# Performance work log

Measured on AMD Instinct MI355X. Metric: run time of the kernel, lower is better.

The kernel has to match this reference:

```python
import jax, jax.numpy as jnp
import numpy as np

N, C, E, H = 50000, 128, 1_600_000, 32
JITTER = 1e-20


def _lin(k, fan_in, fan_out):
    return jax.random.normal(k, (fan_in, fan_out), jnp.float32) / np.sqrt(fan_in)


def setup_inputs() -> dict:
    key = jax.random.key(0)
    ks = jax.random.split(key, 20)
    x = jax.random.normal(ks[0], (N, C), jnp.float32)
    edge_index = jax.random.randint(ks[1], (2, E), 0, N, dtype=jnp.int64)
    inp = {"x": x, "edge_index": edge_index}
    # actor params
    inp["aW"] = _lin(ks[2], C, C); inp["ab"] = jnp.zeros((C,), jnp.float32)
    inp["a1W"] = _lin(ks[3], C, H); inp["a1b"] = jnp.zeros((H,), jnp.float32)
    inp["a2W"] = _lin(ks[4], H, H); inp["a2b"] = jnp.zeros((H,), jnp.float32)
    inp["a3W"] = _lin(ks[5], H, 2); inp["a3b"] = jnp.zeros((2,), jnp.float32)
    # critic params
    inp["cW"] = _lin(ks[6], C, C); inp["cb"] = jnp.zeros((C,), jnp.float32)
    inp["c1W"] = _lin(ks[7], C, H); inp["c1b"] = jnp.zeros((H,), jnp.float32)
    inp["c2W"] = _lin(ks[8], H, H); inp["c2b"] = jnp.zeros((H,), jnp.float32)
    inp["c3W"] = _lin(ks[9], H, 2); inp["c3b"] = jnp.zeros((2,), jnp.float32)
    return inp


def gcn_conv(x, src, dst, W, b):
    """Standard PyG GCNConv: add self-loops, symmetric degree norm, X@W, scatter-add, +bias."""
    n = x.shape[0]
    loop = jnp.arange(n)
    s = jnp.concatenate([src, loop])  # [E+N]
    d = jnp.concatenate([dst, loop])
    deg = jax.ops.segment_sum(jnp.ones_like(d, jnp.float32), d, num_segments=n)
    dinv = jnp.where(deg > 0, jax.lax.rsqrt(deg), 0.0)
    norm = dinv[s] * dinv[d]                     # [E+N]
    h = x @ W                                    # [N, C]
    agg = jax.ops.segment_sum(h[s] * norm[:, None], d, num_segments=n)
    return agg + b


def reference(x, edge_index, aW, ab, a1W, a1b, a2W, a2b, a3W, a3b,
              cW, cb, c1W, c1b, c2W, c2b, c3W, c3b):
    src, dst = edge_index[0], edge_index[1]
    # actor
    h = jax.nn.relu(gcn_conv(x, src, dst, aW, ab)) + x
    h = jax.nn.relu(h @ a1W + a1b)
    h = jax.nn.relu(h @ a2W + a2b)
    a = h @ a3W + a3b                            # [N, 2]
    concentration = jax.nn.softplus(a[:, 0]) + JITTER
    p = jax.nn.softplus(a[:, 1])
    action2_probs = p / jnp.sum(p)
    # critic
    hc = jax.nn.relu(gcn_conv(x, src, dst, cW, cb)) + x
    hc = jnp.sum(hc, axis=0)                     # [C]
    hc = jax.nn.relu(hc @ c1W + c1b)
    hc = jax.nn.relu(hc @ c2W + c2b)
    value = hc @ c3W + c3b                       # [2]
    return (concentration, value, action2_probs)
```

## Files before the change

kernel.cpp:

```cpp
#include <hip/hip_runtime.h>
#include <hip/hip_bf16.h>
#include <hip/hip_fp16.h>
#include <math.h>

#define C 128
#define BCAP 12288

using half8x = __attribute__((ext_vector_type(8))) _Float16;
using half4x = __attribute__((ext_vector_type(4))) _Float16;
using f32x4  = __attribute__((ext_vector_type(4))) float;

__device__ inline float4 h4_to_f4(uint2 u) {
    __half2 p0 = *(__half2*)&u.x;
    __half2 p1 = *(__half2*)&u.y;
    float2 f0 = __half22float2(p0), f1 = __half22float2(p1);
    return make_float4(f0.x, f0.y, f1.x, f1.y);
}

__device__ inline float softplusf(float v) {
    return (v > 20.f) ? v : log1pf(expf(v));
}

__global__ __launch_bounds__(256) void initk(unsigned* gcur, float* colsum, float* pSum) {
    int t = threadIdx.x;
    gcur[t] = 0u;
    if (t < 128) colsum[t] = 0.f;
    if (t == 128) pSum[0] = 0.f;
}

__global__ __launch_bounds__(256) void wtk(const float* __restrict__ aW, const float* __restrict__ cW,
                                           const float* __restrict__ a1W,
                                           __half* __restrict__ wt, __half* __restrict__ a1wt) {
    int idx = blockIdx.x * 256 + threadIdx.x;
    if (idx < 32768) {
        int y = idx >> 14, r = idx & 16383;
        int k = r >> 7, n = r & 127;
        const float* W = y ? cW : aW;
        wt[((size_t)y << 14) + n * 128 + k] = __float2half(W[k * 128 + n]);
    } else if (idx < 36864) {
        int r = idx - 32768;
        int k = r >> 5, n = r & 31;
        a1wt[n * 128 + k] = __float2half(a1W[k * 32 + n]);
    }
}

__global__ __launch_bounds__(256) void bink(const int* __restrict__ ei,
                                            unsigned* __restrict__ gcur,
                                            unsigned* __restrict__ gstage,
                                            int E, int NBKT) {
    __shared__ unsigned raw[6400];
    __shared__ unsigned image[6400];
    __shared__ unsigned cnt[256];
    __shared__ unsigned pref[256];
    __shared__ unsigned cur[256];
    __shared__ unsigned gb[256];
    int t = threadIdx.x, b = blockIdx.x;
    int elo = (int)((long long)b * E / 256);
    int ehi = (int)((long long)(b + 1) * E / 256);
    int n = ehi - elo;

    for (int i = t; i < n; i += 256) {
        int d = __builtin_nontemporal_load(ei + E + elo + i);
        int s = __builtin_nontemporal_load(ei + elo + i);
        raw[i] = (unsigned)s | ((unsigned)(d & 255) << 16) | ((unsigned)(d >> 8) << 24);
    }
    cnt[t] = 0u; cur[t] = 0u;
    __syncthreads();
    for (int i = t; i < n; i += 256) atomicAdd(&cnt[raw[i] >> 24], 1u);
    __syncthreads();
    pref[t] = cnt[t];
    __syncthreads();
    for (int off = 1; off < 256; off <<= 1) {
        unsigned add = (t >= off) ? pref[t - off] : 0u;
        __syncthreads();
        pref[t] += add;
        __syncthreads();
    }
    gb[t] = (t < NBKT && cnt[t]) ? atomicAdd(&gcur[t], cnt[t]) : 0u;
    __syncthreads();
    for (int i = t; i < n; i += 256) {
        unsigned v = raw[i];
        unsigned B = v >> 24;
        unsigned pos = (pref[B] - cnt[B]) + atomicAdd(&cur[B], 1u);
        image[pos] = v & 0xFFFFFFu;
    }
    __syncthreads();
    int wv = t >> 6, lane = t & 63;
    for (int B = wv; B < NBKT; B += 4) {
        unsigned c = cnt[B];
        if (!c) continue;
        unsigned eb = pref[B] - c;
        unsigned gbase = gb[B];
        unsigned c2 = (gbase < BCAP) ? ((c < BCAP - gbase) ? c : BCAP - gbase) : 0u;
        for (unsigned i = lane; i < c2; i += 64)
            gstage[(size_t)B * BCAP + gbase + i] = image[eb + i];
    }
}

__global__ void bktscank(const unsigned* __restrict__ gcur, unsigned* __restrict__ bktbase, int NBKT) {
    __shared__ unsigned tmp[256];
    int t = threadIdx.x;
    unsigned g = (t < NBKT) ? gcur[t] : 0u;
    unsigned v = (g < BCAP) ? g : BCAP;
    tmp[t] = v;
    __syncthreads();
    for (int off = 1; off < 256; off <<= 1) {
        unsigned add = (t >= off) ? tmp[t - off] : 0u;
        __syncthreads();
        tmp[t] += add;
        __syncthreads();
    }
    if (t < NBKT) bktbase[t] = tmp[t] - v;
}

__global__ __launch_bounds__(256) void placek(const unsigned* __restrict__ gstage,
                                              const unsigned* __restrict__ gcur,
                                              const unsigned* __restrict__ bktbase,
                                              int* __restrict__ rowptr, float* __restrict__ dinv,
                                              int* __restrict__ col, int N, int NBKT) {
    __shared__ unsigned image[BCAP];
    __shared__ unsigned cnt[256];
    __shared__ unsigned pref[256];
    __shared__ unsigned cur[256];
    int B = blockIdx.x, t = threadIdx.x;
    unsigned g = gcur[B];
    unsigned m = (g < BCAP) ? g : BCAP;
    unsigned base = bktbase[B];
    const unsigned* st = gstage + (size_t)B * BCAP;

    cnt[t] = 0u; cur[t] = 0u;
    __syncthreads();
    for (unsigned i = t; i < m; i += 256) atomicAdd(&cnt[(st[i] >> 16) & 255u], 1u);
    __syncthreads();
    pref[t] = cnt[t];
    __syncthreads();
    for (int off = 1; off < 256; off <<= 1) {
        unsigned add = (t >= off) ? pref[t - off] : 0u;
        __syncthreads();
        pref[t] += add;
        __syncthreads();
    }
    int d = B * 256 + t;
    if (d < N) {
        rowptr[d] = (int)(base + pref[t] - cnt[t]);
        dinv[d] = rsqrtf((float)(cnt[t] + 1u));
    }
    if (B == NBKT - 1 && t == 0) rowptr[N] = (int)(base + m);
    for (unsigned i = t; i < m; i += 256) {
        unsigned v = st[i];
        unsigned dl = (v >> 16) & 255u;
        unsigned pos = (pref[dl] - cnt[dl]) + atomicAdd(&cur[dl], 1u);
        image[pos] = v & 0xFFFFu;
    }
    __syncthreads();
    for (unsigned i = t; i < m; i += 256) col[base + i] = (int)image[i];
}

__global__ __launch_bounds__(256) void xhk(const float* __restrict__ x, const float* __restrict__ dinv,
                                           __half* __restrict__ xh, __half* __restrict__ x16, int N) {
    int i = blockIdx.x * 256 + threadIdx.x;
    if (i >= N * 64) return;
    int node = i >> 6, fp = (i & 63) * 2;
    float w = dinv[node];
    float2 f = *(const float2*)&x[(size_t)node * C + fp];
    __half2 h = __floats2half2_rn(f.x * w, f.y * w);
    __half2 hx = __floats2half2_rn(f.x, f.y);
    *(unsigned*)&xh[(size_t)node * C + fp] = *(unsigned*)&h;
    *(unsigned*)&x16[(size_t)node * C + fp] = *(unsigned*)&hx;
}

__global__ __launch_bounds__(256) void gatherk(const int* __restrict__ col,
                                               const int* __restrict__ rowptr,
                                               const __half* __restrict__ xh,
                                               const float* __restrict__ dinv,
                                               __half* __restrict__ gg, int N) {
    __shared__ int snb[4][64];
    int t = threadIdx.x;
    int wid = t >> 6, lane = t & 63;
    int d = blockIdx.x * 4 + wid;
    if (d >= N) return;
    int beg = rowptr[d], end = rowptr[d + 1];
    int half = lane >> 5, sub = lane & 31;
    int f = sub * 4;

    float a0 = 0.f, a1 = 0.f, a2 = 0.f, a3 = 0.f;

    for (int c = beg; c < end; c += 64) {
        if (c + lane < end) snb[wid][lane] = col[c + lane];
        int n = end - c; if (n > 64) n = 64;
        int j = 0;
        for (; j + 3 < n; j += 4) {
            size_t i0 = (size_t)snb[wid][j + half] * C + f;
            size_t i1 = (size_t)snb[wid][j + 2 + half] * C + f;
            float4 v0 = h4_to_f4(*(const uint2*)&xh[i0]);
            float4 v1 = h4_to_f4(*(const uint2*)&xh[i1]);
            a0 += v0.x + v1.x;
            a1 += v0.y + v1.y;
            a2 += v0.z + v1.z;
            a3 += v0.w + v1.w;
        }
        for (; j < n; j += 2) {
            if (j + half < n) {
                float4 v = h4_to_f4(*(const uint2*)&xh[(size_t)snb[wid][j + half] * C + f]);
                a0 += v.x; a1 += v.y; a2 += v.z; a3 += v.w;
            }
        }
    }
    a0 += __shfl_xor(a0, 32, 64);
    a1 += __shfl_xor(a1, 32, 64);
    a2 += __shfl_xor(a2, 32, 64);
    a3 += __shfl_xor(a3, 32, 64);

    if (half == 0) {
        float4 s4 = h4_to_f4(*(const uint2*)&xh[(size_t)d * C + f]);
        float dv = dinv[d];
        __half2 h0 = __floats2half2_rn((a0 + s4.x) * dv, (a1 + s4.y) * dv);
        __half2 h1 = __floats2half2_rn((a2 + s4.z) * dv, (a3 + s4.w) * dv);
        uint2 u; u.x = *(unsigned*)&h0; u.y = *(unsigned*)&h1;
        *(uint2*)&gg[(size_t)d * C + f] = u;
    }
}

__global__ __launch_bounds__(256) void gemm2k(const __half* __restrict__ gg,
                                              const __half* __restrict__ wt,
                                              const __half* __restrict__ a1wt,
                                              const float* __restrict__ ab, const float* __restrict__ cb,
                                              const __half* __restrict__ x16,
                                              const float* __restrict__ a1b,
                                              const float* __restrict__ a2W, const float* __restrict__ a2b,
                                              const float* __restrict__ a3W, const float* __restrict__ a3b,
                                              float* __restrict__ scratch,
                                              float* __restrict__ out, float* __restrict__ pSum, int N) {
    __shared__ char As[16384];
    __shared__ char Act[16384];
    __shared__ char Aux[8448];
    _Float16* w2t = (_Float16*)Aux;
    _Float16* h1b = (_Float16*)(Aux + 2560);
    float* w3s    = (float*)(Aux + 7680);
    float* scol   = (float*)(Aux + 7936);

    const int row0 = blockIdx.x * 64;
    const int t = threadIdx.x;

#pragma unroll
    for (int i = 0; i < 4; ++i) {
        int c = t + i * 256;
        int row = c >> 4, cb16 = (c & 15) * 16;
        int grow = row0 + row;
        uint4 u = make_uint4(0u, 0u, 0u, 0u);
        if (grow < N) u = *(const uint4*)&gg[(size_t)grow * C + (c & 15) * 8];
        *(uint4*)(As + row * 256 + (cb16 ^ ((row & 7) << 4))) = u;
    }
#pragma unroll
    for (int i = 0; i < 4; ++i) {
        int idx = t + i * 256;
        int k = idx >> 5, n = idx & 31;
        w2t[n * 40 + k] = (_Float16)a2W[idx];
    }
    if (t < 64) w3s[t] = a3W[t];
    __syncthreads();

    int wv = t >> 6, l = t & 63;
    int lm = l & 15, lk = l >> 4;
    int koffB = lk * 16;
    int koffH = lk * 8;

    const __half* WA = wt;
    const __half* WC = wt + 16384;

#pragma unroll
    for (int nc2 = 0; nc2 < 2; ++nc2) {
        const int nc = wv * 2 + nc2;
        const __half* wpA = WA + (nc * 16 + lm) * 128;
        const __half* wpC = WC + (nc * 16 + lm) * 128;
        half8x bfA[4], bfC[4];
#pragma unroll
        for (int kc = 0; kc < 4; ++kc) {
            bfA[kc] = *(const half8x*)(wpA + kc * 32 + koffH);
            bfC[kc] = *(const half8x*)(wpC + kc * 32 + koffH);
        }
        float4 bvA = *(const float4*)&ab[nc * 16 + lk * 4];
        float4 bvC = *(const float4*)&cb[nc * 16 + lk * 4];
        float v0 = 0.f, v1 = 0.f, v2 = 0.f, v3 = 0.f;

#pragma unroll
        for (int rg = 0; rg < 4; ++rg) {
            int rowA = rg * 16 + lm;
            int grow = row0 + rowA;
            bool valid = grow < N;
            int sw = (rowA & 7) << 4;
            const char* rp = As + rowA * 256;
            f32x4 accA = {0.f, 0.f, 0.f, 0.f};
            f32x4 accC = {0.f, 0.f, 0.f, 0.f};
#pragma unroll
            for (int kc = 0; kc < 4; ++kc) {
                half8x afr = *(const half8x*)(rp + ((kc * 64 + koffB) ^ sw));
                accA = __builtin_amdgcn_mfma_f32_16x16x32_f16(bfA[kc], afr, accA, 0, 0, 0);
                accC = __builtin_amdgcn_mfma_f32_16x16x32_f16(bfC[kc], afr, accC, 0, 0, 0);
            }
            half4x xq = {};
            if (valid) xq = *(const half4x*)&x16[(size_t)grow * C + nc * 16 + lk * 4];
            half4x hv = { (_Float16)(valid ? fmaxf(accA[0] + bvA.x, 0.f) + (float)xq[0] : 0.f),
                          (_Float16)(valid ? fmaxf(accA[1] + bvA.y, 0.f) + (float)xq[1] : 0.f),
                          (_Float16)(valid ? fmaxf(accA[2] + bvA.z, 0.f) + (float)xq[2] : 0.f),
                          (_Float16)(valid ? fmaxf(accA[3] + bvA.w, 0.f) + (float)xq[3] : 0.f) };
            *(half4x*)(Act + rowA * 256 + ((nc * 32 + lk * 8) ^ sw)) = hv;
            v0 += valid ? fmaxf(accC[0] + bvC.x, 0.f) + (float)xq[0] : 0.f;
            v1 += valid ? fmaxf(accC[1] + bvC.y, 0.f) + (float)xq[1] : 0.f;
            v2 += valid ? fmaxf(accC[2] + bvC.z, 0.f) + (float)xq[2] : 0.f;
            v3 += valid ? fmaxf(accC[3] + bvC.w, 0.f) + (float)xq[3] : 0.f;
        }
        v0 += __shfl_xor(v0, 1, 64); v0 += __shfl_xor(v0, 2, 64);
        v0 += __shfl_xor(v0, 4, 64); v0 += __shfl_xor(v0, 8, 64);
        v1 += __shfl_xor(v1, 1, 64); v1 += __shfl_xor(v1, 2, 64);
        v1 += __shfl_xor(v1, 4, 64); v1 += __shfl_xor(v1, 8, 64);
        v2 += __shfl_xor(v2, 1, 64); v2 += __shfl_xor(v2, 2, 64);
        v2 += __shfl_xor(v2, 4, 64); v2 += __shfl_xor(v2, 8, 64);
        v3 += __shfl_xor(v3, 1, 64); v3 += __shfl_xor(v3, 2, 64);
        v3 += __shfl_xor(v3, 4, 64); v3 += __shfl_xor(v3, 8, 64);
        if (lm == 0)
            *(float4*)&scol[nc * 16 + lk * 4] = make_float4(v0, v1, v2, v3);
    }
    __syncthreads();

    if (t < 128)
        scratch[(size_t)blockIdx.x * 128 + t] = scol[t];

    const int rowM = wv * 16 + lm;
    const int growM = row0 + rowM;
    const bool validM = growM < N;
    const int swM = (rowM & 7) << 4;

    half8x a1f[4];
    {
        const char* rp = Act + rowM * 256;
#pragma unroll
        for (int kc = 0; kc < 4; ++kc)
            a1f[kc] = *(const half8x*)(rp + ((kc * 64 + koffB) ^ swM));
    }
#pragma unroll
    for (int ct = 0; ct < 2; ++ct) {
        const __half* ap = a1wt + (ct * 16 + lm) * 128;
        f32x4 acc1 = {0.f, 0.f, 0.f, 0.f};
#pragma unroll
        for (int kc = 0; kc < 4; ++kc) {
            half8x bq = *(const half8x*)(ap + kc * 32 + koffH);
            acc1 = __builtin_amdgcn_mfma_f32_16x16x32_f16(bq, a1f[kc], acc1, 0, 0, 0);
        }
        float4 b1v = *(const float4*)&a1b[ct * 16 + lk * 4];
        half4x h = { (_Float16)fmaxf(acc1[0] + b1v.x, 0.f),
                     (_Float16)fmaxf(acc1[1] + b1v.y, 0.f),
                     (_Float16)fmaxf(acc1[2] + b1v.z, 0.f),
                     (_Float16)fmaxf(acc1[3] + b1v.w, 0.f) };
        *(half4x*)((char*)h1b + rowM * 80 + ct * 32 + lk * 8) = h;
    }

    half4x alo = *(const half4x*)((char*)h1b + rowM * 80 + lk * 16);
    half4x ahi = *(const half4x*)((char*)h1b + rowM * 80 + lk * 16 + 8);
    half8x a2f = __builtin_shufflevector(alo, ahi, 0, 1, 2, 3, 4, 5, 6, 7);
    float p0 = 0.f, p1 = 0.f;
#pragma unroll
    for (int ct = 0; ct < 2; ++ct) {
        half4x blo = *(const half4x*)((char*)w2t + (ct * 16 + lm) * 80 + lk * 16);
        half4x bhi = *(const half4x*)((char*)w2t + (ct * 16 + lm) * 80 + lk * 16 + 8);
        half8x b2f = __builtin_shufflevector(blo, bhi, 0, 1, 2, 3, 4, 5, 6, 7);
        f32x4 acc2 = {0.f, 0.f, 0.f, 0.f};
        acc2 = __builtin_amdgcn_mfma_f32_16x16x32_f16(b2f, a2f, acc2, 0, 0, 0);
        float4 b2v = *(const float4*)&a2b[ct * 16 + lk * 4];
#pragma unroll
        for (int j = 0; j < 4; ++j) {
            int f = ct * 16 + lk * 4 + j;
            float h2v = fmaxf(acc2[j] + (&b2v.x)[j], 0.f);
            float2 w3 = *(const float2*)&w3s[f * 2];
            p0 += h2v * w3.x;
            p1 += h2v * w3.y;
        }
    }
    p0 += __shfl_xor(p0, 16, 64); p0 += __shfl_xor(p0, 32, 64);
    p1 += __shfl_xor(p1, 16, 64); p1 += __shfl_xor(p1, 32, 64);
    float wave_psum = 0.f;
    if (lk == 0 && validM) {
        float s0 = softplusf(p0 + a3b[0]);
        float s1 = softplusf(p1 + a3b[1]);
        out[growM] = s0 + 1e-20f;
        out[(size_t)N + 2 + growM] = s1;
        wave_psum = s1;
    }
    wave_psum += __shfl_xor(wave_psum, 1, 64);
    wave_psum += __shfl_xor(wave_psum, 2, 64);
    wave_psum += __shfl_xor(wave_psum, 4, 64);
    wave_psum += __shfl_xor(wave_psum, 8, 64);
    wave_psum += __shfl_xor(wave_psum, 16, 64);
    wave_psum += __shfl_xor(wave_psum, 32, 64);
    if (l == 0) atomicAdd(pSum, wave_psum);
}

__global__ __launch_bounds__(128) void csredk(const float* __restrict__ scratch, float* __restrict__ colsum, int nblk) {
    int t = threadIdx.x;
    float s = 0.f;
    for (int b = blockIdx.x; b < nblk; b += gridDim.x)
        s += scratch[(size_t)b * 128 + t];
    atomicAdd(&colsum[t], s);
}

__global__ void critick(const float* __restrict__ colsum,
                        const float* __restrict__ c1W, const float* __restrict__ c1b,
                        const float* __restrict__ c2W, const float* __restrict__ c2b,
                        const float* __restrict__ c3W, const float* __restrict__ c3b,
                        float* __restrict__ out, int N) {
    __shared__ float s1[32], s2[32];
    int t = threadIdx.x;
    if (t < 32) {
        float acc = c1b[t];
        for (int k = 0; k < 128; ++k) acc += colsum[k] * c1W[k * 32 + t];
        s1[t] = fmaxf(acc, 0.f);
    }
    __syncthreads();
    if (t < 32) {
        float acc = c2b[t];
        for (int k = 0; k < 32; ++k) acc += s1[k] * c2W[k * 32 + t];
        s2[t] = fmaxf(acc, 0.f);
    }
    __syncthreads();
    if (t < 2) {
        float acc = c3b[t];
        for (int k = 0; k < 32; ++k) acc += s2[k] * c3W[k * 2 + t];
        out[(size_t)N + t] = acc;
    }
}

__global__ __launch_bounds__(256) void normk(float* __restrict__ out, const float* __restrict__ pSum, int N) {
    int i = blockIdx.x * 256 + threadIdx.x;
    if (i < N) out[(size_t)N + 2 + i] /= pSum[0];
}

extern "C" void kernel_launch(void* const* d_in, const int* in_sizes, int n_in,
                              void* d_out, int out_size, void* d_ws, size_t ws_size,
                              hipStream_t stream) {
    const float* x   = (const float*)d_in[0];
    const int* ei    = (const int*)d_in[1];
    const float* aW  = (const float*)d_in[2];
    const float* ab  = (const float*)d_in[3];
    const float* a1W = (const float*)d_in[4];
    const float* a1b = (const float*)d_in[5];
    const float* a2W = (const float*)d_in[6];
    const float* a2b = (const float*)d_in[7];
    const float* a3W = (const float*)d_in[8];
    const float* a3b = (const float*)d_in[9];
    const float* cW  = (const float*)d_in[10];
    const float* cb  = (const float*)d_in[11];
    const float* c1W = (const float*)d_in[12];
    const float* c1b = (const float*)d_in[13];
    const float* c2W = (const float*)d_in[14];
    const float* c2b = (const float*)d_in[15];
    const float* c3W = (const float*)d_in[16];
    const float* c3b = (const float*)d_in[17];

    const int N = in_sizes[0] / C;
    const int E = in_sizes[1] / 2;
    const int NBKT = (N + 255) / 256;
    const int nblk64 = (N + 63) / 64;
    float* out = (float*)d_out;

    char* ws = (char*)d_ws;
    size_t off = 0;
    auto alloc = [&](size_t bytes) {
        size_t o = off;
        off = (off + bytes + 255) & ~(size_t)255;
        return (void*)(ws + o);
    };
    unsigned* gcur    = (unsigned*)alloc(256 * 4);
    unsigned* bktbase = (unsigned*)alloc(256 * 4);
    unsigned* gstage  = (unsigned*)alloc((size_t)NBKT * BCAP * 4);
    int* rowptr       = (int*)alloc((size_t)(N + 1) * 4);
    float* dinv       = (float*)alloc((size_t)N * 4);
    int* colidx       = (int*)alloc((size_t)E * 4);
    __half* xh        = (__half*)alloc((size_t)N * C * 2);
    __half* x16       = (__half*)alloc((size_t)N * C * 2);
    __half* gg        = (__half*)alloc((size_t)N * C * 2);
    __half* wt        = (__half*)alloc(2 * 16384 * 2);
    __half* a1wt      = (__half*)alloc(4096 * 2);
    float* scratch    = (float*)alloc((size_t)nblk64 * 128 * 4);
    float* colsum     = (float*)alloc(128 * 4);
    float* pSum       = (float*)alloc(4);

    initk<<<1, 256, 0, stream>>>(gcur, colsum, pSum);
    wtk<<<144, 256, 0, stream>>>(aW, cW, a1W, wt, a1wt);
    bink<<<256, 256, 0, stream>>>(ei, gcur, gstage, E, NBKT);
    bktscank<<<1, 256, 0, stream>>>(gcur, bktbase, NBKT);
    placek<<<NBKT, 256, 0, stream>>>(gstage, gcur, bktbase, rowptr, dinv, colidx, N, NBKT);
    xhk<<<(N * 64 + 255) / 256, 256, 0, stream>>>(x, dinv, xh, x16, N);
    gatherk<<<(N + 3) / 4, 256, 0, stream>>>(colidx, rowptr, xh, dinv, gg, N);
    gemm2k<<<nblk64, 256, 0, stream>>>(gg, wt, a1wt, ab, cb, x16,
                                       a1b, a2W, a2b, a3W, a3b,
                                       scratch, out, pSum, N);
    csredk<<<8, 128, 0, stream>>>(scratch, colsum, nblk64);
    critick<<<1, 64, 0, stream>>>(colsum, c1W, c1b, c2W, c2b, c3W, c3b, out, N);
    normk<<<(N + 255) / 256, 256, 0, stream>>>(out, pSum, N);
}
```

Before: 217.7 us.

## Split gather features into four 32-column slabs and prefetch residual in GEMM

The scaled half-precision features are stored as four slabs of 32 columns each. The gather kernel now runs a second grid dimension over slabs, so each slab (about 3.2 MB) is more likely to stay in cache during random neighbor reads. Each wave handles 8 neighbors at a time with 8 lanes per neighbor and reduces the partial sums with shuffles. Separately, the GEMM kernel loads the residual x16 values into registers before the shared-memory fill, which hides their latency. The cost is that edge indices and rowptr are read four times, and each random read is now only 64 bytes per neighbor.

```diff
diff --git a/kernel.cpp b/kernel.cpp
--- a/kernel.cpp
+++ b/kernel.cpp
@@ -157,7 +157,7 @@
 }
 
 __global__ __launch_bounds__(256) void xhk(const float* __restrict__ x, const float* __restrict__ dinv,
-                                           __half* __restrict__ xh, __half* __restrict__ x16, int N) {
+                                           __half* __restrict__ xhS, __half* __restrict__ x16, int N) {
     int i = blockIdx.x * 256 + threadIdx.x;
     if (i >= N * 64) return;
     int node = i >> 6, fp = (i & 63) * 2;
@@ -165,59 +165,49 @@
     float2 f = *(const float2*)&x[(size_t)node * C + fp];
     __half2 h = __floats2half2_rn(f.x * w, f.y * w);
     __half2 hx = __floats2half2_rn(f.x, f.y);
-    *(unsigned*)&xh[(size_t)node * C + fp] = *(unsigned*)&h;
+    int s = fp >> 5, off = fp & 31;
+    *(unsigned*)&xhS[((size_t)s * N + node) * 32 + off] = *(unsigned*)&h;
     *(unsigned*)&x16[(size_t)node * C + fp] = *(unsigned*)&hx;
 }
 
 __global__ __launch_bounds__(256) void gatherk(const int* __restrict__ col,
                                                const int* __restrict__ rowptr,
-                                               const __half* __restrict__ xh,
+                                               const __half* __restrict__ xhS,
                                                const float* __restrict__ dinv,
                                                __half* __restrict__ gg, int N) {
     __shared__ int snb[4][64];
     int t = threadIdx.x;
     int wid = t >> 6, lane = t & 63;
     int d = blockIdx.x * 4 + wid;
+    int p = blockIdx.y;
     if (d >= N) return;
+    const __half* xs = xhS + (size_t)p * N * 32;
     int beg = rowptr[d], end = rowptr[d + 1];
-    int half = lane >> 5, sub = lane & 31;
-    int f = sub * 4;
+    int g = lane >> 3, q = lane & 7;
+    int f = q * 4;
 
     float a0 = 0.f, a1 = 0.f, a2 = 0.f, a3 = 0.f;
 
     for (int c = beg; c < end; c += 64) {
         if (c + lane < end) snb[wid][lane] = col[c + lane];
         int n = end - c; if (n > 64) n = 64;
-        int j = 0;
-        for (; j + 3 < n; j += 4) {
-            size_t i0 = (size_t)snb[wid][j + half] * C + f;
-            size_t i1 = (size_t)snb[wid][j + 2 + half] * C + f;
-            float4 v0 = h4_to_f4(*(const uint2*)&xh[i0]);
-            float4 v1 = h4_to_f4(*(const uint2*)&xh[i1]);
-            a0 += v0.x + v1.x;
-            a1 += v0.y + v1.y;
-            a2 += v0.z + v1.z;
-            a3 += v0.w + v1.w;
+        for (int j = g; j < n; j += 8) {
+            float4 v = h4_to_f4(*(const uint2*)&xs[(size_t)snb[wid][j] * 32 + f]);
+            a0 += v.x; a1 += v.y; a2 += v.z; a3 += v.w;
         }
-        for (; j < n; j += 2) {
-            if (j + half < n) {
-                float4 v = h4_to_f4(*(const uint2*)&xh[(size_t)snb[wid][j + half] * C + f]);
-                a0 += v.x; a1 += v.y; a2 += v.z; a3 += v.w;
-            }
-        }
-    }
-    a0 += __shfl_xor(a0, 32, 64);
-    a1 += __shfl_xor(a1, 32, 64);
-    a2 += __shfl_xor(a2, 32, 64);
-    a3 += __shfl_xor(a3, 32, 64);
-
-    if (half == 0) {
-        float4 s4 = h4_to_f4(*(const uint2*)&xh[(size_t)d * C + f]);
+    }
+    a0 += __shfl_xor(a0, 8, 64);  a0 += __shfl_xor(a0, 16, 64);  a0 += __shfl_xor(a0, 32, 64);
+    a1 += __shfl_xor(a1, 8, 64);  a1 += __shfl_xor(a1, 16, 64);  a1 += __shfl_xor(a1, 32, 64);
+    a2 += __shfl_xor(a2, 8, 64);  a2 += __shfl_xor(a2, 16, 64);  a2 += __shfl_xor(a2, 32, 64);
+    a3 += __shfl_xor(a3, 8, 64);  a3 += __shfl_xor(a3, 16, 64);  a3 += __shfl_xor(a3, 32, 64);
+
+    if (g == 0) {
+        float4 s4 = h4_to_f4(*(const uint2*)&xs[(size_t)d * 32 + f]);
         float dv = dinv[d];
         __half2 h0 = __floats2half2_rn((a0 + s4.x) * dv, (a1 + s4.y) * dv);
         __half2 h1 = __floats2half2_rn((a2 + s4.z) * dv, (a3 + s4.w) * dv);
         uint2 u; u.x = *(unsigned*)&h0; u.y = *(unsigned*)&h1;
-        *(uint2*)&gg[(size_t)d * C + f] = u;
+        *(uint2*)&gg[(size_t)d * C + p * 32 + f] = u;
     }
 }
 
@@ -241,6 +231,22 @@
 
     const int row0 = blockIdx.x * 64;
     const int t = threadIdx.x;
+    const int wv = t >> 6, l = t & 63;
+    const int lm = l & 15, lk = l >> 4;
+    const int koffB = lk * 16;
+    const int koffH = lk * 8;
+
+    uint2 xpre[4][2];
+#pragma unroll
+    for (int rg = 0; rg < 4; ++rg) {
+        int grow = row0 + rg * 16 + lm;
+#pragma unroll
+        for (int nc2 = 0; nc2 < 2; ++nc2) {
+            int nc = wv * 2 + nc2;
+            xpre[rg][nc2] = (grow < N) ? *(const uint2*)&x16[(size_t)grow * C + nc * 16 + lk * 4]
+                                       : make_uint2(0u, 0u);
+        }
+    }
 
 #pragma unroll
     for (int i = 0; i < 4; ++i) {
@@ -259,11 +265,6 @@
     }
     if (t < 64) w3s[t] = a3W[t];
     __syncthreads();
-
-    int wv = t >> 6, l = t & 63;
-    int lm = l & 15, lk = l >> 4;
-    int koffB = lk * 16;
-    int koffH = lk * 8;
 
     const __half* WA = wt;
     const __half* WC = wt + 16384;
@@ -298,8 +299,7 @@
                 accA = __builtin_amdgcn_mfma_f32_16x16x32_f16(bfA[kc], afr, accA, 0, 0, 0);
                 accC = __builtin_amdgcn_mfma_f32_16x16x32_f16(bfC[kc], afr, accC, 0, 0, 0);
             }
-            half4x xq = {};
-            if (valid) xq = *(const half4x*)&x16[(size_t)grow * C + nc * 16 + lk * 4];
+            half4x xq = *(half4x*)&xpre[rg][nc2];
             half4x hv = { (_Float16)(valid ? fmaxf(accA[0] + bvA.x, 0.f) + (float)xq[0] : 0.f),
                           (_Float16)(valid ? fmaxf(accA[1] + bvA.y, 0.f) + (float)xq[1] : 0.f),
                           (_Float16)(valid ? fmaxf(accA[2] + bvA.z, 0.f) + (float)xq[2] : 0.f),
@@ -475,7 +475,7 @@
     int* rowptr       = (int*)alloc((size_t)(N + 1) * 4);
     float* dinv       = (float*)alloc((size_t)N * 4);
     int* colidx       = (int*)alloc((size_t)E * 4);
-    __half* xh        = (__half*)alloc((size_t)N * C * 2);
+    __half* xhS       = (__half*)alloc((size_t)N * C * 2);
     __half* x16       = (__half*)alloc((size_t)N * C * 2);
     __half* gg        = (__half*)alloc((size_t)N * C * 2);
     __half* wt        = (__half*)alloc(2 * 16384 * 2);
@@ -489,8 +489,8 @@
     bink<<<256, 256, 0, stream>>>(ei, gcur, gstage, E, NBKT);
     bktscank<<<1, 256, 0, stream>>>(gcur, bktbase, NBKT);
     placek<<<NBKT, 256, 0, stream>>>(gstage, gcur, bktbase, rowptr, dinv, colidx, N, NBKT);
-    xhk<<<(N * 64 + 255) / 256, 256, 0, stream>>>(x, dinv, xh, x16, N);
-    gatherk<<<(N + 3) / 4, 256, 0, stream>>>(colidx, rowptr, xh, dinv, gg, N);
+    xhk<<<(N * 64 + 255) / 256, 256, 0, stream>>>(x, dinv, xhS, x16, N);
+    gatherk<<<dim3((N + 3) / 4, 4), 256, 0, stream>>>(colidx, rowptr, xhS, dinv, gg, N);
     gemm2k<<<nblk64, 256, 0, stream>>>(gg, wt, a1wt, ab, cb, x16,
                                        a1b, a2W, a2b, a3W, a3b,
                                        scratch, out, pSum, N);
```

Measured after the change: 246.9 us (median of 2 runs). +13.4%, slower.
